# Kernel optimization log

Measured on AMD Instinct MI355X. Metric: run time of the kernel, lower is better.

## Reference

```python
import jax, jax.numpy as jnp
import numpy as np

IN_F = 4096
OUT_F = 4096
RANK = 16
ALPHA = 32
BLOCK = 64  # quantization blocksize along in_features
SCALING = ALPHA / RANK


def setup_inputs() -> dict:
    key = jax.random.key(0)
    k1, k2, k3, k4, k5, k6 = jax.random.split(key, 6)
    x = jax.random.normal(k1, (4, 2048, IN_F), dtype=jnp.float32)
    # int4 codes stored with +8 offset, values in [0, 16)
    q_codes = jax.random.randint(k2, (OUT_F, IN_F), 0, 16, dtype=jnp.int32)
    # per-(row, block) dequant scales
    scales = jax.random.uniform(k3, (OUT_F, IN_F // BLOCK), dtype=jnp.float32) * 0.02
    bias = jax.random.normal(k4, (OUT_F,), dtype=jnp.float32) * 0.02
    lora_A = jax.random.normal(k5, (RANK, IN_F), dtype=jnp.float32) * (1.0 / np.sqrt(IN_F))
    lora_B = jax.random.normal(k6, (OUT_F, RANK), dtype=jnp.float32) * 0.02
    return {"x": x, "q_codes": q_codes, "scales": scales, "bias": bias,
            "lora_A": lora_A, "lora_B": lora_B}


def _dequant(q_codes, scales):
    # [O, I] int4 codes (offset by 8) -> fp32 weight via blockwise scales
    O, I = q_codes.shape
    c = (q_codes.astype(jnp.float32) - 8.0).reshape(O, I // BLOCK, BLOCK)
    return (c * scales[:, :, None]).reshape(O, I)


def reference(x, q_codes, scales, bias, lora_A, lora_B):
    w = _dequant(q_codes, scales)                      # [O, I]
    base = jnp.einsum('bsi,oi->bso', x, w) + bias      # dequant GEMM + bias
    # LoRA branch: dropout(p=0) is identity; x @ (B@A).T == (x @ A.T) @ B.T
    lora = jnp.einsum('bsr,or->bso', jnp.einsum('bsi,ri->bsr', x, lora_A), lora_B)
    return base + lora * SCALING
```

## Files before the change

### kernel.cpp

```cpp
#include <hip/hip_runtime.h>
#include <hip/hip_bf16.h>

#define IN_F   4096
#define OUT_F  4096
#define RANK   16
#define M_TOK  8192
#define SCALING 2.0f

typedef __attribute__((ext_vector_type(8))) short short8;
typedef __attribute__((ext_vector_type(4))) float f32x4;
typedef __attribute__((ext_vector_type(4))) float fvec4;
typedef __attribute__((ext_vector_type(4))) int   ivec4;
typedef __attribute__((ext_vector_type(4))) unsigned int uvec4;

__global__ __launch_bounds__(256) void cvt_x(const float* __restrict__ x,
                                             __hip_bfloat16* __restrict__ xb) {
    const size_t nvec = (size_t)M_TOK * IN_F / 8;
    const size_t stride = (size_t)gridDim.x * 256;
    for (size_t idx = (size_t)blockIdx.x * 256 + threadIdx.x; idx < nvec; idx += stride) {
        const size_t i = idx * 8;
        fvec4 a = __builtin_nontemporal_load((const fvec4*)(x + i));
        fvec4 b = __builtin_nontemporal_load((const fvec4*)(x + i + 4));
        union { uvec4 u; __hip_bfloat16 h[8]; } p;
        p.h[0] = __float2bfloat16(a.x);
        p.h[1] = __float2bfloat16(a.y);
        p.h[2] = __float2bfloat16(a.z);
        p.h[3] = __float2bfloat16(a.w);
        p.h[4] = __float2bfloat16(b.x);
        p.h[5] = __float2bfloat16(b.y);
        p.h[6] = __float2bfloat16(b.z);
        p.h[7] = __float2bfloat16(b.w);
        *(uvec4*)(xb + i) = p.u;
    }
}

__global__ __launch_bounds__(256) void dequant_lora(const int* __restrict__ q,
                                                    const float* __restrict__ sc,
                                                    const float* __restrict__ lA,
                                                    const float* __restrict__ lB,
                                                    __hip_bfloat16* __restrict__ W) {
    const int c0 = (blockIdx.x & 3) * 1024 + threadIdx.x * 4;
    const int o0 = (blockIdx.x >> 2) * 16;

    fvec4 a[RANK];
#pragma unroll
    for (int r = 0; r < RANK; ++r)
        a[r] = *(const fvec4*)(lA + (size_t)r * IN_F + c0);

    const float s_base = 0.f; (void)s_base;
#pragma unroll 2
    for (int oo = 0; oo < 16; ++oo) {
        const int o = o0 + oo;
        ivec4 qv = __builtin_nontemporal_load((const ivec4*)(q + (size_t)o * IN_F + c0));
        const float s = sc[o * (IN_F / 64) + (c0 >> 6)];
        const float* lbo = lB + o * RANK;
        float l0 = 0.f, l1 = 0.f, l2 = 0.f, l3 = 0.f;
#pragma unroll
        for (int r = 0; r < RANK; ++r) {
            const float br = lbo[r];
            l0 += br * a[r].x; l1 += br * a[r].y;
            l2 += br * a[r].z; l3 += br * a[r].w;
        }
        union { ushort4 u; __hip_bfloat16 h[4]; } p;
        p.h[0] = __float2bfloat16((float)(qv.x - 8) * s + SCALING * l0);
        p.h[1] = __float2bfloat16((float)(qv.y - 8) * s + SCALING * l1);
        p.h[2] = __float2bfloat16((float)(qv.z - 8) * s + SCALING * l2);
        p.h[3] = __float2bfloat16((float)(qv.w - 8) * s + SCALING * l3);
        *(ushort4*)(W + (size_t)o * IN_F + c0) = p.u;
    }
}


__device__ __forceinline__ void load_lds16(const void* g, void* l) {
    __builtin_amdgcn_global_load_lds(
        (const __attribute__((address_space(1))) unsigned int*)g,
        (__attribute__((address_space(3))) unsigned int*)l, 16, 0, 0);
}

#define MFMA_BF16 __builtin_amdgcn_mfma_f32_16x16x32_bf16

__global__ __launch_bounds__(512, 2) void gemm256_8ph(const __hip_bfloat16* __restrict__ A,
                                                      const __hip_bfloat16* __restrict__ B,
                                                      const float* __restrict__ bias,
                                                      float* __restrict__ C) {
    extern __shared__ __align__(16) char lds[];

    const int tid  = threadIdx.x;
    const int lane = tid & 63;
    const int wave = tid >> 6;

    const int xcd = blockIdx.x & 7;
    const int w64 = blockIdx.x >> 3;
    const int tm  = (xcd >> 1) * 8 + (w64 >> 3);
    const int tn  = (xcd & 1) * 8 + (w64 & 7);

    const __hip_bfloat16* Ab = A + (size_t)tm * 256 * IN_F;
    const __hip_bfloat16* Bb = B + (size_t)tn * 256 * IN_F;

    const int    c0   = ((lane & 3) * 8) ^ ((lane >= 32) ? 16 : 0);
    const size_t off0 = (size_t)((wave >> 1) * 16 + (lane >> 2)) * IN_F
                      + (size_t)((wave & 1) * 32 + c0);

    const int flo = (lane & 15) * 64 + (((lane >> 4) * 16) ^ ((lane & 8) << 2));

    const int ah = wave >> 2;
    const int bh = (wave >> 1) & 1;
    const int bs = (wave & 1) * 4;

#define STAGE2(gp, lo) do {                                               \
        load_lds16((gp) + off0,             lds + (lo) + wave * 1024);    \
        load_lds16((gp) + off0 + 64 * IN_F, lds + (lo) + (8 + wave) * 1024); \
    } while (0)

    STAGE2(Bb,                    32768);
    STAGE2(Bb + 128 * IN_F,       49152);
    STAGE2(Ab,                    0);
    STAGE2(Ab + 128 * IN_F,       16384);
    STAGE2(Bb + 64,               65536 + 32768);
    STAGE2(Bb + 64 + 128 * IN_F,  65536 + 49152);
    asm volatile("s_waitcnt vmcnt(4)" ::: "memory");
    __builtin_amdgcn_s_barrier();

    short8 aF[4][2], bA[2][2], bB[2][2];
    f32x4 acc[8][4] = {};

    for (int t = 0; t < 64; ++t) {
        const int cb = (t & 1) << 16;
        const int nb = cb ^ 65536;
        const int t1 = ((t + 1) & 63) << 6;
        const int t2 = ((t + 2) & 63) << 6;
        const int aO = cb + ah * 16384;
        const int bO = cb + 32768 + bh * 16384;

#pragma unroll
        for (int i = 0; i < 4; ++i)
#pragma unroll
            for (int kk = 0; kk < 2; ++kk)
                aF[i][kk] = *(const short8*)(lds + aO + (i * 2 + kk) * 1024 + flo);
#pragma unroll
        for (int j = 0; j < 2; ++j)
#pragma unroll
            for (int kk = 0; kk < 2; ++kk)
                bA[j][kk] = *(const short8*)(lds + bO + ((bs + j) * 2 + kk) * 1024 + flo);
        STAGE2(Ab + t1, nb);
        __builtin_amdgcn_s_barrier();
        __builtin_amdgcn_s_setprio(1);
#pragma unroll
        for (int i = 0; i < 4; ++i)
#pragma unroll
            for (int j = 0; j < 2; ++j)
#pragma unroll
                for (int kk = 0; kk < 2; ++kk)
                    acc[i][j] = MFMA_BF16(aF[i][kk], bA[j][kk], acc[i][j], 0, 0, 0);
        __builtin_amdgcn_s_setprio(0);
        __builtin_amdgcn_s_barrier();

#pragma unroll
        for (int j = 0; j < 2; ++j)
#pragma unroll
            for (int kk = 0; kk < 2; ++kk)
                bB[j][kk] = *(const short8*)(lds + bO + ((bs + 2 + j) * 2 + kk) * 1024 + flo);
        STAGE2(Ab + 128 * IN_F + t1, nb + 16384);
        __builtin_amdgcn_s_barrier();
        __builtin_amdgcn_s_setprio(1);
#pragma unroll
        for (int i = 0; i < 4; ++i)
#pragma unroll
            for (int j = 0; j < 2; ++j)
#pragma unroll
                for (int kk = 0; kk < 2; ++kk)
                    acc[i][2 + j] = MFMA_BF16(aF[i][kk], bB[j][kk], acc[i][2 + j], 0, 0, 0);
        __builtin_amdgcn_s_setprio(0);
        __builtin_amdgcn_s_barrier();

#pragma unroll
        for (int i = 0; i < 4; ++i)
#pragma unroll
            for (int kk = 0; kk < 2; ++kk)
                aF[i][kk] = *(const short8*)(lds + aO + ((4 + i) * 2 + kk) * 1024 + flo);
        STAGE2(Bb + t2, cb + 32768);
        __builtin_amdgcn_s_barrier();
        __builtin_amdgcn_s_setprio(1);
#pragma unroll
        for (int i = 0; i < 4; ++i)
#pragma unroll
            for (int j = 0; j < 2; ++j)
#pragma unroll
                for (int kk = 0; kk < 2; ++kk)
                    acc[4 + i][2 + j] = MFMA_BF16(aF[i][kk], bB[j][kk], acc[4 + i][2 + j], 0, 0, 0);
        __builtin_amdgcn_s_setprio(0);
        __builtin_amdgcn_s_barrier();

        STAGE2(Bb + 128 * IN_F + t2, cb + 49152);
        asm volatile("s_waitcnt vmcnt(4)" ::: "memory");
        __builtin_amdgcn_s_barrier();
        __builtin_amdgcn_s_setprio(1);
#pragma unroll
        for (int i = 0; i < 4; ++i)
#pragma unroll
            for (int j = 0; j < 2; ++j)
#pragma unroll
                for (int kk = 0; kk < 2; ++kk)
                    acc[4 + i][j] = MFMA_BF16(aF[i][kk], bA[j][kk], acc[4 + i][j], 0, 0, 0);
        __builtin_amdgcn_s_setprio(0);
        __builtin_amdgcn_s_barrier();
    }
    asm volatile("s_waitcnt vmcnt(0)" ::: "memory");

    const int qd = lane >> 4;
    const int cl = lane & 15;
    const size_t m_base = (size_t)tm * 256 + (size_t)ah * 128;
    const int    n_base = tn * 256 + (wave & 3) * 64;
#pragma unroll
    for (int fn = 0; fn < 4; ++fn) {
        const int n = n_base + fn * 16 + cl;
        const float bv = bias[n];
#pragma unroll
        for (int fm = 0; fm < 8; ++fm) {
            const size_t m0 = m_base + fm * 16 + qd * 4;
#pragma unroll
            for (int r = 0; r < 4; ++r)
                __builtin_nontemporal_store(acc[fm][fn][r] + bv,
                                            &C[(m0 + r) * OUT_F + n]);
        }
    }
#undef STAGE2
}

extern "C" void kernel_launch(void* const* d_in, const int* in_sizes, int n_in,
                              void* d_out, int out_size, void* d_ws, size_t ws_size,
                              hipStream_t stream) {
    const float* x    = (const float*)d_in[0];
    const int*   qc   = (const int*)d_in[1];
    const float* sc   = (const float*)d_in[2];
    const float* bias = (const float*)d_in[3];
    const float* lA   = (const float*)d_in[4];
    const float* lB   = (const float*)d_in[5];
    float* out = (float*)d_out;

    __hip_bfloat16* xb = (__hip_bfloat16*)d_ws;
    __hip_bfloat16* wb = xb + (size_t)M_TOK * IN_F;

    static bool attr_done = false;
    if (!attr_done) {
        (void)hipFuncSetAttribute((const void*)gemm256_8ph,
                                  hipFuncAttributeMaxDynamicSharedMemorySize, 131072);
        attr_done = true;
    }

    cvt_x<<<2048, 256, 0, stream>>>(x, xb);
    dequant_lora<<<1024, 256, 0, stream>>>(qc, sc, lA, lB, wb);
    gemm256_8ph<<<dim3(512), dim3(512), 131072, stream>>>(xb, wb, bias, out);
}
```

Measured before the change: 487.5 us.

## Merge x-convert and dequant kernels into one launch; unroll GEMM loop by two

Combines the fp32-to-bf16 activation conversion and the int4 dequant+LoRA weight build into one kernel, with odd blocks doing conversion and even blocks doing dequant. This removes a launch and lets the two memory-bound phases overlap. The dequant path now loads all eight code rows before computing, for more memory-level parallelism. The GEMM main loop is unrolled by two with precomputed LDS read pointers and global base pointers, which makes buffer offsets compile-time constants and cuts address arithmetic.

```diff
diff --git a/kernel.cpp b/kernel.cpp
--- a/kernel.cpp
+++ b/kernel.cpp
@@ -13,60 +13,73 @@
 typedef __attribute__((ext_vector_type(4))) int   ivec4;
 typedef __attribute__((ext_vector_type(4))) unsigned int uvec4;
 
-__global__ __launch_bounds__(256) void cvt_x(const float* __restrict__ x,
-                                             __hip_bfloat16* __restrict__ xb) {
-    const size_t nvec = (size_t)M_TOK * IN_F / 8;
-    const size_t stride = (size_t)gridDim.x * 256;
-    for (size_t idx = (size_t)blockIdx.x * 256 + threadIdx.x; idx < nvec; idx += stride) {
-        const size_t i = idx * 8;
-        fvec4 a = __builtin_nontemporal_load((const fvec4*)(x + i));
-        fvec4 b = __builtin_nontemporal_load((const fvec4*)(x + i + 4));
-        union { uvec4 u; __hip_bfloat16 h[8]; } p;
-        p.h[0] = __float2bfloat16(a.x);
-        p.h[1] = __float2bfloat16(a.y);
-        p.h[2] = __float2bfloat16(a.z);
-        p.h[3] = __float2bfloat16(a.w);
-        p.h[4] = __float2bfloat16(b.x);
-        p.h[5] = __float2bfloat16(b.y);
-        p.h[6] = __float2bfloat16(b.z);
-        p.h[7] = __float2bfloat16(b.w);
-        *(uvec4*)(xb + i) = p.u;
-    }
-}
-
-__global__ __launch_bounds__(256) void dequant_lora(const int* __restrict__ q,
-                                                    const float* __restrict__ sc,
-                                                    const float* __restrict__ lA,
-                                                    const float* __restrict__ lB,
-                                                    __hip_bfloat16* __restrict__ W) {
-    const int c0 = (blockIdx.x & 3) * 1024 + threadIdx.x * 4;
-    const int o0 = (blockIdx.x >> 2) * 16;
-
-    fvec4 a[RANK];
-#pragma unroll
-    for (int r = 0; r < RANK; ++r)
-        a[r] = *(const fvec4*)(lA + (size_t)r * IN_F + c0);
-
-    const float s_base = 0.f; (void)s_base;
-#pragma unroll 2
-    for (int oo = 0; oo < 16; ++oo) {
-        const int o = o0 + oo;
-        ivec4 qv = __builtin_nontemporal_load((const ivec4*)(q + (size_t)o * IN_F + c0));
-        const float s = sc[o * (IN_F / 64) + (c0 >> 6)];
-        const float* lbo = lB + o * RANK;
-        float l0 = 0.f, l1 = 0.f, l2 = 0.f, l3 = 0.f;
-#pragma unroll
-        for (int r = 0; r < RANK; ++r) {
-            const float br = lbo[r];
-            l0 += br * a[r].x; l1 += br * a[r].y;
-            l2 += br * a[r].z; l3 += br * a[r].w;
+__global__ __launch_bounds__(256) void prep2(const float* __restrict__ x,
+                                             __hip_bfloat16* __restrict__ xb,
+                                             const int* __restrict__ q,
+                                             const float* __restrict__ sc,
+                                             const float* __restrict__ lA,
+                                             const float* __restrict__ lB,
+                                             __hip_bfloat16* __restrict__ W) {
+    const int bid = blockIdx.x;
+    const int tid = threadIdx.x;
+    if (bid & 1) {
+        const size_t base   = (size_t)(bid >> 1) * 256 + tid;
+        const size_t stride = (size_t)2048 * 256;
+#pragma unroll
+        for (int it = 0; it < 8; ++it) {
+            const size_t i = (base + (size_t)it * stride) * 8;
+            fvec4 a = __builtin_nontemporal_load((const fvec4*)(x + i));
+            fvec4 b = __builtin_nontemporal_load((const fvec4*)(x + i + 4));
+            union { uvec4 u; __hip_bfloat16 h[8]; } p;
+            p.h[0] = __float2bfloat16(a.x);
+            p.h[1] = __float2bfloat16(a.y);
+            p.h[2] = __float2bfloat16(a.z);
+            p.h[3] = __float2bfloat16(a.w);
+            p.h[4] = __float2bfloat16(b.x);
+            p.h[5] = __float2bfloat16(b.y);
+            p.h[6] = __float2bfloat16(b.z);
+            p.h[7] = __float2bfloat16(b.w);
+            *(uvec4*)(xb + i) = p.u;
         }
-        union { ushort4 u; __hip_bfloat16 h[4]; } p;
-        p.h[0] = __float2bfloat16((float)(qv.x - 8) * s + SCALING * l0);
-        p.h[1] = __float2bfloat16((float)(qv.y - 8) * s + SCALING * l1);
-        p.h[2] = __float2bfloat16((float)(qv.z - 8) * s + SCALING * l2);
-        p.h[3] = __float2bfloat16((float)(qv.w - 8) * s + SCALING * l3);
-        *(ushort4*)(W + (size_t)o * IN_F + c0) = p.u;
+    } else {
+        const int id = bid >> 1;
+        const int c0 = (id & 3) * 1024 + tid * 4;
+        const int o0 = (id >> 2) * 8;
+
+        ivec4 qv[8];
+#pragma unroll
+        for (int oo = 0; oo < 8; ++oo)
+            qv[oo] = __builtin_nontemporal_load(
+                (const ivec4*)(q + (size_t)(o0 + oo) * IN_F + c0));
+
+        float sv[8];
+#pragma unroll
+        for (int oo = 0; oo < 8; ++oo)
+            sv[oo] = sc[(o0 + oo) * (IN_F / 64) + (c0 >> 6)];
+
+        fvec4 a[RANK];
+#pragma unroll
+        for (int r = 0; r < RANK; ++r)
+            a[r] = *(const fvec4*)(lA + (size_t)r * IN_F + c0);
+
+#pragma unroll
+        for (int oo = 0; oo < 8; ++oo) {
+            const float* lbo = lB + (size_t)(o0 + oo) * RANK;
+            float l0 = 0.f, l1 = 0.f, l2 = 0.f, l3 = 0.f;
+#pragma unroll
+            for (int r = 0; r < RANK; ++r) {
+                const float br = lbo[r];
+                l0 += br * a[r].x; l1 += br * a[r].y;
+                l2 += br * a[r].z; l3 += br * a[r].w;
+            }
+            const float s = sv[oo];
+            union { ushort4 u; __hip_bfloat16 h[4]; } p;
+            p.h[0] = __float2bfloat16((float)(qv[oo].x - 8) * s + SCALING * l0);
+            p.h[1] = __float2bfloat16((float)(qv[oo].y - 8) * s + SCALING * l1);
+            p.h[2] = __float2bfloat16((float)(qv[oo].z - 8) * s + SCALING * l2);
+            p.h[3] = __float2bfloat16((float)(qv[oo].w - 8) * s + SCALING * l3);
+            *(ushort4*)(W + (size_t)(o0 + oo) * IN_F + c0) = p.u;
+        }
     }
 }
 
@@ -101,109 +114,123 @@
     const size_t off0 = (size_t)((wave >> 1) * 16 + (lane >> 2)) * IN_F
                       + (size_t)((wave & 1) * 32 + c0);
 
+    const __hip_bfloat16* qA0 = Ab + off0;
+    const __hip_bfloat16* qA1 = Ab + (size_t)128 * IN_F + off0;
+    const __hip_bfloat16* qB0 = Bb + off0;
+    const __hip_bfloat16* qB1 = Bb + (size_t)128 * IN_F + off0;
+
     const int flo = (lane & 15) * 64 + (((lane >> 4) * 16) ^ ((lane & 8) << 2));
 
     const int ah = wave >> 2;
     const int bh = (wave >> 1) & 1;
     const int bs = (wave & 1) * 4;
 
-#define STAGE2(gp, lo) do {                                               \
-        load_lds16((gp) + off0,             lds + (lo) + wave * 1024);    \
-        load_lds16((gp) + off0 + 64 * IN_F, lds + (lo) + (8 + wave) * 1024); \
+    const char* aRd[2] = { lds + ah * 16384 + flo,
+                           lds + 65536 + ah * 16384 + flo };
+    const char* bRd[2] = { lds + 32768 + bh * 16384 + bs * 2048 + flo,
+                           lds + 65536 + 32768 + bh * 16384 + bs * 2048 + flo };
+
+    const int wv1024 = wave * 1024;
+
+#define STAGE2(ps, te, LO) do {                                             \
+        const __hip_bfloat16* g_ = (ps) + (te);                             \
+        load_lds16(g_,              lds + (LO) + wv1024);                   \
+        load_lds16(g_ + 64 * IN_F,  lds + (LO) + 8192 + wv1024);            \
     } while (0)
 
-    STAGE2(Bb,                    32768);
-    STAGE2(Bb + 128 * IN_F,       49152);
-    STAGE2(Ab,                    0);
-    STAGE2(Ab + 128 * IN_F,       16384);
-    STAGE2(Bb + 64,               65536 + 32768);
-    STAGE2(Bb + 64 + 128 * IN_F,  65536 + 49152);
+    STAGE2(qB0, 0,  32768);
+    STAGE2(qB1, 0,  49152);
+    STAGE2(qA0, 0,  0);
+    STAGE2(qA1, 0,  16384);
+    STAGE2(qB0, 64, 65536 + 32768);
+    STAGE2(qB1, 64, 65536 + 49152);
     asm volatile("s_waitcnt vmcnt(4)" ::: "memory");
     __builtin_amdgcn_s_barrier();
 
-    short8 aF[4][2], bA[2][2], bB[2][2];
+    short8 aF[4][2], bAf[2][2], bBf[2][2];
     f32x4 acc[8][4] = {};
 
-    for (int t = 0; t < 64; ++t) {
-        const int cb = (t & 1) << 16;
-        const int nb = cb ^ 65536;
-        const int t1 = ((t + 1) & 63) << 6;
-        const int t2 = ((t + 2) & 63) << 6;
-        const int aO = cb + ah * 16384;
-        const int bO = cb + 32768 + bh * 16384;
-
-#pragma unroll
-        for (int i = 0; i < 4; ++i)
-#pragma unroll
-            for (int kk = 0; kk < 2; ++kk)
-                aF[i][kk] = *(const short8*)(lds + aO + (i * 2 + kk) * 1024 + flo);
-#pragma unroll
-        for (int j = 0; j < 2; ++j)
-#pragma unroll
-            for (int kk = 0; kk < 2; ++kk)
-                bA[j][kk] = *(const short8*)(lds + bO + ((bs + j) * 2 + kk) * 1024 + flo);
-        STAGE2(Ab + t1, nb);
-        __builtin_amdgcn_s_barrier();
-        __builtin_amdgcn_s_setprio(1);
-#pragma unroll
-        for (int i = 0; i < 4; ++i)
-#pragma unroll
-            for (int j = 0; j < 2; ++j)
-#pragma unroll
-                for (int kk = 0; kk < 2; ++kk)
-                    acc[i][j] = MFMA_BF16(aF[i][kk], bA[j][kk], acc[i][j], 0, 0, 0);
-        __builtin_amdgcn_s_setprio(0);
-        __builtin_amdgcn_s_barrier();
-
-#pragma unroll
-        for (int j = 0; j < 2; ++j)
-#pragma unroll
-            for (int kk = 0; kk < 2; ++kk)
-                bB[j][kk] = *(const short8*)(lds + bO + ((bs + 2 + j) * 2 + kk) * 1024 + flo);
-        STAGE2(Ab + 128 * IN_F + t1, nb + 16384);
-        __builtin_amdgcn_s_barrier();
-        __builtin_amdgcn_s_setprio(1);
-#pragma unroll
-        for (int i = 0; i < 4; ++i)
-#pragma unroll
-            for (int j = 0; j < 2; ++j)
-#pragma unroll
-                for (int kk = 0; kk < 2; ++kk)
-                    acc[i][2 + j] = MFMA_BF16(aF[i][kk], bB[j][kk], acc[i][2 + j], 0, 0, 0);
-        __builtin_amdgcn_s_setprio(0);
-        __builtin_amdgcn_s_barrier();
-
-#pragma unroll
-        for (int i = 0; i < 4; ++i)
-#pragma unroll
-            for (int kk = 0; kk < 2; ++kk)
-                aF[i][kk] = *(const short8*)(lds + aO + ((4 + i) * 2 + kk) * 1024 + flo);
-        STAGE2(Bb + t2, cb + 32768);
-        __builtin_amdgcn_s_barrier();
-        __builtin_amdgcn_s_setprio(1);
-#pragma unroll
-        for (int i = 0; i < 4; ++i)
-#pragma unroll
-            for (int j = 0; j < 2; ++j)
-#pragma unroll
-                for (int kk = 0; kk < 2; ++kk)
-                    acc[4 + i][2 + j] = MFMA_BF16(aF[i][kk], bB[j][kk], acc[4 + i][2 + j], 0, 0, 0);
-        __builtin_amdgcn_s_setprio(0);
-        __builtin_amdgcn_s_barrier();
-
-        STAGE2(Bb + 128 * IN_F + t2, cb + 49152);
-        asm volatile("s_waitcnt vmcnt(4)" ::: "memory");
-        __builtin_amdgcn_s_barrier();
-        __builtin_amdgcn_s_setprio(1);
-#pragma unroll
-        for (int i = 0; i < 4; ++i)
-#pragma unroll
-            for (int j = 0; j < 2; ++j)
-#pragma unroll
-                for (int kk = 0; kk < 2; ++kk)
-                    acc[4 + i][j] = MFMA_BF16(aF[i][kk], bA[j][kk], acc[4 + i][j], 0, 0, 0);
-        __builtin_amdgcn_s_setprio(0);
-        __builtin_amdgcn_s_barrier();
+#define TILE(T, CBI) do {                                                          \
+        const int t1e = (((T) + 1) & 63) << 6;        \
+        const int t2e = (((T) + 2) & 63) << 6;                                     \
+                           \
+        _Pragma("unroll")                                                          \
+        for (int i = 0; i < 4; ++i)                                                \
+            _Pragma("unroll")                                                      \
+            for (int kk = 0; kk < 2; ++kk)                                         \
+                aF[i][kk] = *(const short8*)(aRd[CBI] + (i * 2 + kk) * 1024);      \
+        _Pragma("unroll")                                                          \
+        for (int j = 0; j < 2; ++j)                                                \
+            _Pragma("unroll")                                                      \
+            for (int kk = 0; kk < 2; ++kk)                                         \
+                bAf[j][kk] = *(const short8*)(bRd[CBI] + (j * 2 + kk) * 1024);     \
+        STAGE2(qA0, t1e, ((CBI) ^ 1) * 65536);                                     \
+        __builtin_amdgcn_s_barrier();                                              \
+        __builtin_amdgcn_s_setprio(1);                                             \
+        _Pragma("unroll")                                                          \
+        for (int i = 0; i < 4; ++i)                                                \
+            _Pragma("unroll")                                                      \
+            for (int j = 0; j < 2; ++j)                                            \
+                _Pragma("unroll")                                                  \
+                for (int kk = 0; kk < 2; ++kk)                                     \
+                    acc[i][j] = MFMA_BF16(aF[i][kk], bAf[j][kk], acc[i][j], 0,0,0);\
+        __builtin_amdgcn_s_setprio(0);                                             \
+        __builtin_amdgcn_s_barrier();                                              \
+                           \
+        _Pragma("unroll")                                                          \
+        for (int j = 0; j < 2; ++j)                                                \
+            _Pragma("unroll")                                                      \
+            for (int kk = 0; kk < 2; ++kk)                                         \
+                bBf[j][kk] = *(const short8*)(bRd[CBI] + 4096 + (j*2+kk) * 1024);  \
+        STAGE2(qA1, t1e, ((CBI) ^ 1) * 65536 + 16384);                             \
+        __builtin_amdgcn_s_barrier();                                              \
+        __builtin_amdgcn_s_setprio(1);                                             \
+        _Pragma("unroll")                                                          \
+        for (int i = 0; i < 4; ++i)                                                \
+            _Pragma("unroll")                                                      \
+            for (int j = 0; j < 2; ++j)                                            \
+                _Pragma("unroll")                                                  \
+                for (int kk = 0; kk < 2; ++kk)                                     \
+                    acc[i][2+j] = MFMA_BF16(aF[i][kk], bBf[j][kk], acc[i][2+j],0,0,0);\
+        __builtin_amdgcn_s_setprio(0);                                             \
+        __builtin_amdgcn_s_barrier();                                              \
+                           \
+        _Pragma("unroll")                                                          \
+        for (int i = 0; i < 4; ++i)                                                \
+            _Pragma("unroll")                                                      \
+            for (int kk = 0; kk < 2; ++kk)                                         \
+                aF[i][kk] = *(const short8*)(aRd[CBI] + 8192 + (i*2+kk) * 1024);   \
+        STAGE2(qB0, t2e, (CBI) * 65536 + 32768);               \
+        __builtin_amdgcn_s_barrier();                                              \
+        __builtin_amdgcn_s_setprio(1);                                             \
+        _Pragma("unroll")                                                          \
+        for (int i = 0; i < 4; ++i)                                                \
+            _Pragma("unroll")                                                      \
+            for (int j = 0; j < 2; ++j)                                            \
+                _Pragma("unroll")                                                  \
+                for (int kk = 0; kk < 2; ++kk)                                     \
+                    acc[4+i][2+j] = MFMA_BF16(aF[i][kk], bBf[j][kk], acc[4+i][2+j],0,0,0);\
+        __builtin_amdgcn_s_setprio(0);                                             \
+        __builtin_amdgcn_s_barrier();                                              \
+                           \
+        STAGE2(qB1, t2e, (CBI) * 65536 + 49152);                                   \
+        asm volatile("s_waitcnt vmcnt(4)" ::: "memory");      \
+        __builtin_amdgcn_s_barrier();                          \
+        __builtin_amdgcn_s_setprio(1);                                             \
+        _Pragma("unroll")                                                          \
+        for (int i = 0; i < 4; ++i)                                                \
+            _Pragma("unroll")                                                      \
+            for (int j = 0; j < 2; ++j)                                            \
+                _Pragma("unroll")                                                  \
+                for (int kk = 0; kk < 2; ++kk)                                     \
+                    acc[4+i][j] = MFMA_BF16(aF[i][kk], bAf[j][kk], acc[4+i][j],0,0,0);\
+        __builtin_amdgcn_s_setprio(0);                                             \
+        __builtin_amdgcn_s_barrier();                                              \
+    } while (0)
+
+    for (int tt = 0; tt < 32; ++tt) {
+        TILE(2 * tt,     0);
+        TILE(2 * tt + 1, 1);
     }
     asm volatile("s_waitcnt vmcnt(0)" ::: "memory");
 
@@ -225,6 +252,7 @@
         }
     }
 #undef STAGE2
+#undef TILE
 }
 
 extern "C" void kernel_launch(void* const* d_in, const int* in_sizes, int n_in,
@@ -248,7 +276,6 @@
         attr_done = true;
     }
 
-    cvt_x<<<2048, 256, 0, stream>>>(x, xb);
-    dequant_lora<<<1024, 256, 0, stream>>>(qc, sc, lA, lB, wb);
+    prep2<<<4096, 256, 0, stream>>>(x, xb, qc, sc, lA, lB, wb);
     gemm256_8ph<<<dim3(512), dim3(512), 131072, stream>>>(xb, wb, bias, out);
 }
```

Result: no change. 486.1 us (-0.3%).
